# Kernel optimization log

Measured on AMD Instinct MI355X. Metric: run time of the kernel, lower is better.

Reference implementation:

```python
import jax, jax.numpy as jnp
import numpy as np

NUM_CLASSES = 80
REG_MAX = 16
CLS_W, BOX_W, DFL_W = 1.0, 2.5, 0.5


def _make_anchors(img=640, strides=(8, 16, 32)):
    pts, strs = [], []
    for s in strides:
        n = img // s
        xs = (np.arange(n, dtype=np.float32) + 0.5) * s
        gy, gx = np.meshgrid(xs, xs, indexing='ij')
        pts.append(np.stack([gx.ravel(), gy.ravel()], axis=1))
        strs.append(np.full((n * n, 1), float(s), np.float32))
    return np.concatenate(pts, 0).astype(np.float32), np.concatenate(strs, 0)


def setup_inputs() -> dict:
    key = jax.random.key(0)
    k1, k2, k3, k4, k5 = jax.random.split(key, 5)
    B, G = 16, 20
    ap, st = _make_anchors()  # A = 8400
    A = ap.shape[0]
    cls_scores = jax.random.uniform(k1, (B, A, NUM_CLASSES), dtype=jnp.float32)
    reg_distri = jax.random.normal(k2, (B, A, 4 * (REG_MAX + 1)), dtype=jnp.float32)
    cxcy = jax.random.uniform(k3, (B, G, 2), dtype=jnp.float32) * 560.0 + 40.0
    wh = jax.random.uniform(k4, (B, G, 2), dtype=jnp.float32) * 120.0 + 20.0
    gt_boxes = jnp.concatenate([cxcy - wh * 0.5, cxcy + wh * 0.5], axis=-1)  # xyxy
    gt_labels = jax.random.randint(k5, (B, G), 0, NUM_CLASSES)
    return {"cls_scores": cls_scores, "reg_distri": reg_distri, "gt_boxes": gt_boxes,
            "anchor_points": jnp.asarray(ap), "stride_tensor": jnp.asarray(st),
            "gt_labels": gt_labels}


def _per_image(pred_cls, pred_reg, gt_boxes, gt_labels, anchor_points, stride):
    A, C = pred_cls.shape
    G = gt_boxes.shape[0]
    k = max(min(13, A // max(G, 1)), 3)
    p = jnp.clip(pred_cls, 1e-7, 1.0 - 1e-7)
    centers = (gt_boxes[:, :2] + gt_boxes[:, 2:]) * 0.5                    # [G,2]
    d = jnp.sqrt(jnp.sum((anchor_points[:, None, :] - centers[None]) ** 2, -1))  # [A,G]
    _, topk_idx = jax.lax.top_k(-d.T, k)                                    # [G,k] nearest anchors
    ax = anchor_points[topk_idx]                                            # [G,k,2]
    inside = ((ax[..., 0] >= gt_boxes[:, None, 0]) & (ax[..., 0] <= gt_boxes[:, None, 2]) &
              (ax[..., 1] >= gt_boxes[:, None, 1]) & (ax[..., 1] <= gt_boxes[:, None, 3]))
    any_in = inside.any(-1, keepdims=True)
    assign_k = jnp.where(any_in, inside, jnp.arange(k) < 3)                 # fallback: 3 nearest
    assign = jnp.zeros((G, A), bool).at[jnp.arange(G)[:, None], topk_idx].set(assign_k)
    aT = assign.T                                                           # [A,G]
    fg = aT.any(1)                                                          # [A]
    last_gt = (G - 1) - jnp.argmax(aT[:, ::-1], axis=1)
    target_box = jnp.where(fg[:, None], gt_boxes[last_gt], 0.0)             # [A,4]
    onehot = jax.nn.one_hot(gt_labels, C, dtype=p.dtype)                    # [G,C]
    target_cls = jnp.max(aT[:, :, None].astype(p.dtype) * onehot[None], axis=1)  # [A,C]
    bce = -(target_cls * jnp.log(p) + (1.0 - target_cls) * jnp.log(1.0 - p))
    num_pos = fg.sum().astype(p.dtype)
    pos_w = jnp.minimum(A / jnp.maximum(num_pos, 1.0), 50.0)
    fgf = fg.astype(p.dtype)[:, None]
    pos_loss = jnp.where(num_pos > 0,
                         jnp.sum(bce * fgf) / jnp.maximum(num_pos * C, 1.0) * pos_w, 0.0)
    neg_loss = jnp.sum(bce * (1.0 - fgf)) / jnp.maximum((A - num_pos) * C, 1.0)
    # box decode (DFL expectation) + smooth-L1 on fg anchors
    reg = jax.nn.softmax(pred_reg.reshape(A, 4, REG_MAX + 1), axis=-1)
    proj = jnp.arange(REG_MAX + 1, dtype=p.dtype)
    dist = jnp.sum(reg * proj, axis=-1)                                     # [A,4]
    s = stride[:, 0]
    pb = jnp.stack([anchor_points[:, 0] - dist[:, 0] * s,
                    anchor_points[:, 1] - dist[:, 1] * s,
                    anchor_points[:, 0] + dist[:, 2] * s,
                    anchor_points[:, 1] + dist[:, 3] * s], axis=-1)
    diff = pb - target_box
    ad = jnp.abs(diff)
    sl1 = jnp.where(ad < 1.0, 0.5 * diff * diff, ad - 0.5)
    box_loss = jnp.where(num_pos > 0,
                         jnp.sum(sl1 * fgf) / jnp.maximum(num_pos * 4.0, 1.0), 0.0)
    return pos_loss + neg_loss, box_loss


def reference(cls_scores, reg_distri, gt_boxes, anchor_points, stride_tensor, gt_labels):
    cls_l, box_l = jax.vmap(
        lambda pc, pr, gb, gl: _per_image(pc, pr, gb, gl, anchor_points, stride_tensor)
    )(cls_scores, reg_distri, gt_boxes, gt_labels)
    loss_cls = cls_l.mean() * CLS_W
    loss_box = box_l.mean() * BOX_W
    return loss_cls + loss_box  # loss_dfl is identically 0 in the original
```

## Files before the change

kernel.cpp:

```cpp
#include <hip/hip_runtime.h>
#include <hip/hip_bf16.h>
#include <cfloat>

#define C_NUM 80
#define REG_MAXP1 17
#define NS 33
#define MAXA 8448
#define FG_STRIDE 512

__device__ inline void cand_for_slot(int sc, float cx, float cy, float& v, int& idx)
{
    v = FLT_MAX; idx = 0x7fffffff;
    int loc, w, n, strd, base;
    if (sc < 36)      { loc = sc;      w = 6; n = 80; strd = 8;  base = 0; }
    else if (sc < 52) { loc = sc - 36; w = 4; n = 40; strd = 16; base = 6400; }
    else if (sc < 68) { loc = sc - 52; w = 4; n = 20; strd = 32; base = 8000; }
    else return;
    float inv = 1.0f / (float)strd;
    int ix0 = (int)floorf(cx * inv - 0.5f) - (w / 2 - 1);
    int iy0 = (int)floorf(cy * inv - 0.5f) - (w / 2 - 1);
    int ix = ix0 + loc % w, iy = iy0 + loc / w;
    if (ix < 0 || ix >= n || iy < 0 || iy >= n) return;
    float ax = ((float)ix + 0.5f) * (float)strd;
    float ay = ((float)iy + 0.5f) * (float)strd;
    float dx = ax - cx, dy = ay - cy;
    v = dx * dx + dy * dy;
    idx = base + iy * n + ix;
}

__global__ __launch_bounds__(1024) void assignraster_kernel(const float* __restrict__ gt_boxes,
                              unsigned int* __restrict__ mask,
                              int* __restrict__ fglist,
                              int* __restrict__ npos,
                              float* __restrict__ acc,
                              int A, int G, int k)
{
    __shared__ unsigned int lmask[8400];
    __shared__ int s_cnt;
    int b = blockIdx.x, t = threadIdx.x;
    int wv = t >> 6, lane = t & 63;

    for (int i = t; i < A; i += 1024) lmask[i] = 0u;
    if (t == 0) s_cnt = 0;
    if (t < 3) acc[b * 3 + t] = 0.f;
    __syncthreads();

    for (int g = wv; g < G; g += 16) {
        const float* box = gt_boxes + (size_t)(b * G + g) * 4;
        float x0 = box[0], y0 = box[1], x1 = box[2], y1 = box[3];
        float cx = (x0 + x1) * 0.5f, cy = (y0 + y1) * 0.5f;

        float v0, v1; int i0, i1;
        cand_for_slot(lane,      cx, cy, v0, i0);
        cand_for_slot(lane + 64, cx, cy, v1, i1);

        int my_sel = 0x7fffffff;
        for (int it = 0; it < k; ++it) {
            float lb; int li; bool s0;
            if (v0 < v1 || (v0 == v1 && i0 < i1)) { lb = v0; li = i0; s0 = true; }
            else                                   { lb = v1; li = i1; s0 = false; }
            float rb = lb; int ri = li;
            for (int off = 32; off; off >>= 1) {
                float ov = __shfl_down(rb, off);
                int   oi = __shfl_down(ri, off);
                if (ov < rb || (ov == rb && oi < ri)) { rb = ov; ri = oi; }
            }
            int win = __shfl(ri, 0);
            if (lane == it) my_sel = win;
            if (li == win) {
                if (s0) { v0 = FLT_MAX; i0 = 0x7fffffff; }
                else    { v1 = FLT_MAX; i1 = 0x7fffffff; }
            }
        }

        bool inside = false;
        if (lane < k && my_sel < 0x7fffffff) {
            int idx = my_sel, n, strd, base;
            if (idx < 6400)      { n = 80; strd = 8;  base = 0; }
            else if (idx < 8000) { n = 40; strd = 16; base = 6400; }
            else                 { n = 20; strd = 32; base = 8000; }
            int loc = idx - base;
            float ax = ((float)(loc % n) + 0.5f) * (float)strd;
            float ay = ((float)(loc / n) + 0.5f) * (float)strd;
            inside = (ax >= x0) && (ax <= x1) && (ay >= y0) && (ay <= y1);
        }
        unsigned long long ball = __ballot(inside);
        if (lane < k && my_sel < 0x7fffffff) {
            bool asg = ball ? inside : (lane < 3);
            if (asg) atomicOr(&lmask[my_sel], 1u << g);
        }
    }
    __syncthreads();

    for (int i = t; i < A; i += 1024) {
        unsigned int m = lmask[i];
        mask[(size_t)b * A + i] = m;
        bool fg = (m != 0u);
        unsigned long long bal = __ballot(fg);
        int cnt = __popcll(bal);
        int base = 0;
        if (lane == 0 && cnt) base = atomicAdd(&s_cnt, cnt);
        base = __shfl(base, 0);
        if (fg) {
            int pre = __popcll(bal & ((1ull << lane) - 1ull));
            fglist[b * FG_STRIDE + base + pre] = i | ((31 - __clz(m)) << 16);
        }
    }
    __syncthreads();
    if (t == 0) npos[b] = s_cnt;
}

__global__ __launch_bounds__(256) void assign_kernel(const float* __restrict__ gt_boxes,
                              const float* __restrict__ anchor_points,
                              int* __restrict__ sel,
                              int B, int A, int G, int k)
{
    __shared__ float s_val[4];
    __shared__ int   s_idx[4];
    __shared__ int   s_sel;
    __shared__ int   s_topk[16];
    __shared__ int   s_anyin;

    int bg = blockIdx.x;
    int b = bg / G, g = bg % G;
    const float* box = gt_boxes + (size_t)(b * G + g) * 4;
    float x0 = box[0], y0 = box[1], x1 = box[2], y1 = box[3];
    float cx = (x0 + x1) * 0.5f, cy = (y0 + y1) * 0.5f;

    int t = threadIdx.x;
    float dv[NS];
#pragma unroll
    for (int s = 0; s < NS; ++s) {
        int i = t + s * 256;
        float d = FLT_MAX;
        if (i < A) {
            float dx = anchor_points[2 * i] - cx;
            float dy = anchor_points[2 * i + 1] - cy;
            d = dx * dx + dy * dy;
        }
        dv[s] = d;
    }

    int wid = t >> 6, lane = t & 63;
    for (int it = 0; it < k; ++it) {
        float best = FLT_MAX; int bi = 0x7fffffff;
#pragma unroll
        for (int s = 0; s < NS; ++s) {
            if (dv[s] < best) { best = dv[s]; bi = t + s * 256; }
        }
        for (int off = 32; off; off >>= 1) {
            float ov = __shfl_down(best, off);
            int   oi = __shfl_down(bi, off);
            if (ov < best || (ov == best && oi < bi)) { best = ov; bi = oi; }
        }
        if (lane == 0) { s_val[wid] = best; s_idx[wid] = bi; }
        __syncthreads();
        if (t == 0) {
            float bv = s_val[0]; int bix = s_idx[0];
#pragma unroll
            for (int w = 1; w < 4; ++w) {
                if (s_val[w] < bv || (s_val[w] == bv && s_idx[w] < bix)) { bv = s_val[w]; bix = s_idx[w]; }
            }
            s_sel = bix;
            s_topk[it] = bix;
        }
        __syncthreads();
        int selx = s_sel;
        if ((selx & 255) == t) {
            int slot = selx >> 8;
#pragma unroll
            for (int s = 0; s < NS; ++s) if (s == slot) dv[s] = FLT_MAX;
        }
    }

    if (t == 0) s_anyin = 0;
    __syncthreads();
    bool inside = false; int aidx = -1;
    if (t < k) {
        aidx = s_topk[t];
        float ax = anchor_points[2 * aidx], ay = anchor_points[2 * aidx + 1];
        inside = (ax >= x0) && (ax <= x1) && (ay >= y0) && (ay <= y1);
        if (inside) atomicOr(&s_anyin, 1);
    }
    __syncthreads();
    if (t < k) {
        bool asg = s_anyin ? inside : (t < 3);
        sel[(size_t)bg * 16 + t] = asg ? aidx : -1;
    }
}

__global__ __launch_bounds__(256) void raster_kernel(const int* __restrict__ sel,
                              unsigned int* __restrict__ mask,
                              int* __restrict__ fglist,
                              int* __restrict__ npos,
                              float* __restrict__ acc,
                              int A, int G, int k)
{
    __shared__ unsigned int lmask[MAXA];
    __shared__ int s_cnt;
    int b = blockIdx.x, t = threadIdx.x;

    for (int i = t; i < A; i += 256) lmask[i] = 0u;
    if (t == 0) s_cnt = 0;
    if (t < 3) acc[b * 3 + t] = 0.f;
    __syncthreads();

    for (int i = t; i < G * 16; i += 256) {
        int slot = i & 15;
        if (slot < k) {
            int a = sel[(size_t)(b * G) * 16 + i];
            if (a >= 0) atomicOr(&lmask[a], 1u << (i >> 4));
        }
    }
    __syncthreads();

    for (int i = t; i < A; i += 256) {
        unsigned int m = lmask[i];
        mask[(size_t)b * A + i] = m;
        if (m) {
            int lg = 31 - __clz(m);
            int p = atomicAdd(&s_cnt, 1);
            fglist[b * FG_STRIDE + p] = i | (lg << 16);
        }
    }
    __syncthreads();
    if (t == 0) npos[b] = s_cnt;
}

__global__ __launch_bounds__(256) void clsbox_kernel(const float4* __restrict__ cls,
                           const float* __restrict__ reg,
                           const float* __restrict__ gt_boxes,
                           const float* __restrict__ ap,
                           const float* __restrict__ st,
                           const unsigned int* __restrict__ mask,
                           const int* __restrict__ gt_labels,
                           const int* __restrict__ fglist,
                           const int* __restrict__ npos,
                           float* __restrict__ acc, int A, int G)
{
    const int CQ = C_NUM / 4;
    int b = blockIdx.y;
    int nq = A * CQ;
    const float4* base = cls + (size_t)b * nq;
    const unsigned int* mrow = mask + (size_t)b * A;
    const int* lab = gt_labels + (size_t)b * G;

    float pos = 0.f, neg = 0.f;
    for (int q = blockIdx.x * 256 + threadIdx.x; q < nq; q += gridDim.x * 256) {
        float4 v = base[q];
        unsigned int m = mrow[q / CQ];
        float p0 = fminf(fmaxf(v.x, 1e-7f), 1.0f - 1e-7f);
        float p1 = fminf(fmaxf(v.y, 1e-7f), 1.0f - 1e-7f);
        float p2 = fminf(fmaxf(v.z, 1e-7f), 1.0f - 1e-7f);
        float p3 = fminf(fmaxf(v.w, 1e-7f), 1.0f - 1e-7f);
        if (m) {
            int c0 = (q % CQ) * 4;
            unsigned int tm = 0, mm = m;
            while (mm) {
                int g = __ffs(mm) - 1;
                mm &= mm - 1;
                unsigned int d = (unsigned int)(lab[g] - c0);
                if (d < 4u) tm |= 1u << d;
            }
            pos -= __logf((tm & 1u) ? p0 : 1.0f - p0);
            pos -= __logf((tm & 2u) ? p1 : 1.0f - p1);
            pos -= __logf((tm & 4u) ? p2 : 1.0f - p2);
            pos -= __logf((tm & 8u) ? p3 : 1.0f - p3);
        } else {
            neg -= __logf(1.0f - p0) + __logf(1.0f - p1) + __logf(1.0f - p2) + __logf(1.0f - p3);
        }
    }

    float bx = 0.f;
    int e = blockIdx.x * 256 + threadIdx.x;
    if (e < npos[b]) {
        int ent = fglist[b * FG_STRIDE + e];
        int a = ent & 0xffff;
        int lg = ent >> 16;
        const float* tb = gt_boxes + (size_t)(b * G + lg) * 4;
        const float* r = reg + ((size_t)b * A + a) * (4 * REG_MAXP1);
        float s = st[a];
        float axp = ap[2 * a], ayp = ap[2 * a + 1];
#pragma unroll
        for (int j = 0; j < 4; ++j) {
            const float* rj = r + j * REG_MAXP1;
            float rr[REG_MAXP1];
#pragma unroll
            for (int i = 0; i < REG_MAXP1; ++i) rr[i] = rj[i];
            float mx = rr[0];
#pragma unroll
            for (int i = 1; i < REG_MAXP1; ++i) mx = fmaxf(mx, rr[i]);
            float sum = 0.f, dot = 0.f;
#pragma unroll
            for (int i = 0; i < REG_MAXP1; ++i) {
                float ev = __expf(rr[i] - mx);
                sum += ev; dot += ev * (float)i;
            }
            float dist = dot / sum;
            float pbj = (j < 2) ? ((j == 0 ? axp : ayp) - dist * s)
                                : ((j == 2 ? axp : ayp) + dist * s);
            float df = pbj - tb[j];
            float ad = fabsf(df);
            bx += (ad < 1.0f) ? 0.5f * df * df : ad - 0.5f;
        }
    }

    for (int off = 32; off; off >>= 1) {
        pos += __shfl_down(pos, off);
        neg += __shfl_down(neg, off);
        bx  += __shfl_down(bx, off);
    }
    __shared__ float sp[4], sn[4], sb[4];
    int wid = threadIdx.x >> 6, lane = threadIdx.x & 63;
    if (lane == 0) { sp[wid] = pos; sn[wid] = neg; sb[wid] = bx; }
    __syncthreads();
    if (threadIdx.x == 0) {
        float P = sp[0] + sp[1] + sp[2] + sp[3];
        float N = sn[0] + sn[1] + sn[2] + sn[3];
        float X = sb[0] + sb[1] + sb[2] + sb[3];
        if (P != 0.f) atomicAdd(&acc[b * 3 + 0], P);
        if (N != 0.f) atomicAdd(&acc[b * 3 + 1], N);
        if (X != 0.f) atomicAdd(&acc[b * 3 + 2], X);
    }
}

__global__ void final_kernel(const float* __restrict__ acc,
                             const int* __restrict__ npos,
                             float* __restrict__ out, int B, int A)
{
    if (threadIdx.x == 0 && blockIdx.x == 0) {
        float cls_sum = 0.f, box_sum = 0.f;
        for (int b = 0; b < B; ++b) {
            float np = (float)npos[b];
            float neg = acc[b * 3 + 1] / fmaxf(((float)A - np) * (float)C_NUM, 1.0f);
            float pos = 0.f, box = 0.f;
            if (np > 0.f) {
                float pw = fminf((float)A / fmaxf(np, 1.0f), 50.0f);
                pos = acc[b * 3 + 0] / fmaxf(np * (float)C_NUM, 1.0f) * pw;
                box = acc[b * 3 + 2] / fmaxf(np * 4.0f, 1.0f);
            }
            cls_sum += pos + neg;
            box_sum += box;
        }
        out[0] = cls_sum / (float)B * 1.0f + box_sum / (float)B * 2.5f;
    }
}

extern "C" void kernel_launch(void* const* d_in, const int* in_sizes, int n_in,
                              void* d_out, int out_size, void* d_ws, size_t ws_size,
                              hipStream_t stream)
{
    const float* cls   = (const float*)d_in[0];
    const float* reg   = (const float*)d_in[1];
    const float* gtb   = (const float*)d_in[2];
    const float* ap    = (const float*)d_in[3];
    const float* st    = (const float*)d_in[4];
    const int*   glab  = (const int*)d_in[5];

    int A = in_sizes[3] / 2;
    int B = in_sizes[0] / (A * C_NUM);
    int G = in_sizes[5] / B;
    int k = A / (G > 1 ? G : 1); if (k > 13) k = 13; if (k < 3) k = 3;

    unsigned int* mask = (unsigned int*)d_ws;
    float* acc   = (float*)(mask + (size_t)B * A);
    int*   npos  = (int*)(acc + 3 * B);
    int*   sel   = npos + B;
    int*   fgl   = sel + (size_t)B * G * 16;

    if (A == 8400 && G <= 32) {
        assignraster_kernel<<<B, 1024, 0, stream>>>(gtb, mask, fgl, npos, acc, A, G, k);
    } else {
        assign_kernel<<<B * G, 256, 0, stream>>>(gtb, ap, sel, B, A, G, k);
        raster_kernel<<<B, 256, 0, stream>>>(sel, mask, fgl, npos, acc, A, G, k);
    }

    dim3 g3(128, B);
    clsbox_kernel<<<g3, 256, 0, stream>>>((const float4*)cls, reg, gtb, ap, st,
                                          mask, glab, fgl, npos, acc, A, G);

    final_kernel<<<1, 64, 0, stream>>>(acc, npos, (float*)d_out, B, A);
}
```

Measured before the change: 159.9 us.

## Split cls and box loss into separate kernels, unroll cls loop by two

Splits the fused cls/box kernel into a streaming BCE kernel and a separate foreground box kernel that gives each of the four box sides its own thread. The cls loop now issues two float4 loads per iteration to raise memory-level parallelism. Removing the serial box work from the first blocks of the cls grid avoids a tail where those blocks run longer than the rest. The cost is one extra kernel launch and a second pass to reduce the box loss.

```diff
diff --git a/kernel.cpp b/kernel.cpp
--- a/kernel.cpp
+++ b/kernel.cpp
@@ -227,15 +227,33 @@
     if (t == 0) npos[b] = s_cnt;
 }
 
-__global__ __launch_bounds__(256) void clsbox_kernel(const float4* __restrict__ cls,
-                           const float* __restrict__ reg,
-                           const float* __restrict__ gt_boxes,
-                           const float* __restrict__ ap,
-                           const float* __restrict__ st,
+__device__ inline void bce4(float4 v, unsigned int m, const int* __restrict__ lab,
+                            int c0, float& pos, float& neg)
+{
+    float p0 = fminf(fmaxf(v.x, 1e-7f), 1.0f - 1e-7f);
+    float p1 = fminf(fmaxf(v.y, 1e-7f), 1.0f - 1e-7f);
+    float p2 = fminf(fmaxf(v.z, 1e-7f), 1.0f - 1e-7f);
+    float p3 = fminf(fmaxf(v.w, 1e-7f), 1.0f - 1e-7f);
+    if (m) {
+        unsigned int tm = 0, mm = m;
+        while (mm) {
+            int g = __ffs(mm) - 1;
+            mm &= mm - 1;
+            unsigned int d = (unsigned int)(lab[g] - c0);
+            if (d < 4u) tm |= 1u << d;
+        }
+        pos -= __logf((tm & 1u) ? p0 : 1.0f - p0);
+        pos -= __logf((tm & 2u) ? p1 : 1.0f - p1);
+        pos -= __logf((tm & 4u) ? p2 : 1.0f - p2);
+        pos -= __logf((tm & 8u) ? p3 : 1.0f - p3);
+    } else {
+        neg -= __logf(1.0f - p0) + __logf(1.0f - p1) + __logf(1.0f - p2) + __logf(1.0f - p3);
+    }
+}
+
+__global__ __launch_bounds__(256) void cls_kernel(const float4* __restrict__ cls,
                            const unsigned int* __restrict__ mask,
                            const int* __restrict__ gt_labels,
-                           const int* __restrict__ fglist,
-                           const int* __restrict__ npos,
                            float* __restrict__ acc, int A, int G)
 {
     const int CQ = C_NUM / 4;
@@ -244,82 +262,81 @@
     const float4* base = cls + (size_t)b * nq;
     const unsigned int* mrow = mask + (size_t)b * A;
     const int* lab = gt_labels + (size_t)b * G;
+    int stride = gridDim.x * 256;
 
     float pos = 0.f, neg = 0.f;
-    for (int q = blockIdx.x * 256 + threadIdx.x; q < nq; q += gridDim.x * 256) {
-        float4 v = base[q];
-        unsigned int m = mrow[q / CQ];
-        float p0 = fminf(fmaxf(v.x, 1e-7f), 1.0f - 1e-7f);
-        float p1 = fminf(fmaxf(v.y, 1e-7f), 1.0f - 1e-7f);
-        float p2 = fminf(fmaxf(v.z, 1e-7f), 1.0f - 1e-7f);
-        float p3 = fminf(fmaxf(v.w, 1e-7f), 1.0f - 1e-7f);
-        if (m) {
-            int c0 = (q % CQ) * 4;
-            unsigned int tm = 0, mm = m;
-            while (mm) {
-                int g = __ffs(mm) - 1;
-                mm &= mm - 1;
-                unsigned int d = (unsigned int)(lab[g] - c0);
-                if (d < 4u) tm |= 1u << d;
-            }
-            pos -= __logf((tm & 1u) ? p0 : 1.0f - p0);
-            pos -= __logf((tm & 2u) ? p1 : 1.0f - p1);
-            pos -= __logf((tm & 4u) ? p2 : 1.0f - p2);
-            pos -= __logf((tm & 8u) ? p3 : 1.0f - p3);
-        } else {
-            neg -= __logf(1.0f - p0) + __logf(1.0f - p1) + __logf(1.0f - p2) + __logf(1.0f - p3);
-        }
-    }
-
+    for (int q0 = blockIdx.x * 256 + threadIdx.x; q0 < nq; q0 += 2 * stride) {
+        int q1 = q0 + stride;
+        bool h1 = q1 < nq;
+        float4 va = base[q0];
+        unsigned int ma = mrow[q0 / CQ];
+        float4 vb; unsigned int mb = 0;
+        if (h1) { vb = base[q1]; mb = mrow[q1 / CQ]; }
+        bce4(va, ma, lab, (q0 % CQ) * 4, pos, neg);
+        if (h1) bce4(vb, mb, lab, (q1 % CQ) * 4, pos, neg);
+    }
+
+    for (int off = 32; off; off >>= 1) {
+        pos += __shfl_down(pos, off);
+        neg += __shfl_down(neg, off);
+    }
+    __shared__ float sp[4], sn[4];
+    int wid = threadIdx.x >> 6, lane = threadIdx.x & 63;
+    if (lane == 0) { sp[wid] = pos; sn[wid] = neg; }
+    __syncthreads();
+    if (threadIdx.x == 0) {
+        float P = sp[0] + sp[1] + sp[2] + sp[3];
+        float N = sn[0] + sn[1] + sn[2] + sn[3];
+        if (P != 0.f) atomicAdd(&acc[b * 3 + 0], P);
+        if (N != 0.f) atomicAdd(&acc[b * 3 + 1], N);
+    }
+}
+
+__global__ __launch_bounds__(256) void boxfg_kernel(const float* __restrict__ reg,
+                           const float* __restrict__ gt_boxes,
+                           const float* __restrict__ ap,
+                           const float* __restrict__ st,
+                           const int* __restrict__ fglist,
+                           const int* __restrict__ npos,
+                           float* __restrict__ acc, int A, int G)
+{
+    int b = blockIdx.y;
+    int idx = blockIdx.x * 256 + threadIdx.x;
+    int e = idx >> 2, j = idx & 3;
     float bx = 0.f;
-    int e = blockIdx.x * 256 + threadIdx.x;
     if (e < npos[b]) {
         int ent = fglist[b * FG_STRIDE + e];
         int a = ent & 0xffff;
         int lg = ent >> 16;
-        const float* tb = gt_boxes + (size_t)(b * G + lg) * 4;
-        const float* r = reg + ((size_t)b * A + a) * (4 * REG_MAXP1);
+        float tbj = gt_boxes[(size_t)(b * G + lg) * 4 + j];
+        const float* rj = reg + ((size_t)b * A + a) * (4 * REG_MAXP1) + j * REG_MAXP1;
+        float rr[REG_MAXP1];
+#pragma unroll
+        for (int i = 0; i < REG_MAXP1; ++i) rr[i] = rj[i];
+        float mx = rr[0];
+#pragma unroll
+        for (int i = 1; i < REG_MAXP1; ++i) mx = fmaxf(mx, rr[i]);
+        float sum = 0.f, dot = 0.f;
+#pragma unroll
+        for (int i = 0; i < REG_MAXP1; ++i) {
+            float ev = __expf(rr[i] - mx);
+            sum += ev; dot += ev * (float)i;
+        }
+        float dist = dot / sum;
         float s = st[a];
-        float axp = ap[2 * a], ayp = ap[2 * a + 1];
-#pragma unroll
-        for (int j = 0; j < 4; ++j) {
-            const float* rj = r + j * REG_MAXP1;
-            float rr[REG_MAXP1];
-#pragma unroll
-            for (int i = 0; i < REG_MAXP1; ++i) rr[i] = rj[i];
-            float mx = rr[0];
-#pragma unroll
-            for (int i = 1; i < REG_MAXP1; ++i) mx = fmaxf(mx, rr[i]);
-            float sum = 0.f, dot = 0.f;
-#pragma unroll
-            for (int i = 0; i < REG_MAXP1; ++i) {
-                float ev = __expf(rr[i] - mx);
-                sum += ev; dot += ev * (float)i;
-            }
-            float dist = dot / sum;
-            float pbj = (j < 2) ? ((j == 0 ? axp : ayp) - dist * s)
-                                : ((j == 2 ? axp : ayp) + dist * s);
-            float df = pbj - tb[j];
-            float ad = fabsf(df);
-            bx += (ad < 1.0f) ? 0.5f * df * df : ad - 0.5f;
-        }
-    }
-
-    for (int off = 32; off; off >>= 1) {
-        pos += __shfl_down(pos, off);
-        neg += __shfl_down(neg, off);
-        bx  += __shfl_down(bx, off);
-    }
-    __shared__ float sp[4], sn[4], sb[4];
+        float ac = ap[2 * a + (j & 1)];
+        float pbj = (j < 2) ? (ac - dist * s) : (ac + dist * s);
+        float df = pbj - tbj;
+        float ad = fabsf(df);
+        bx = (ad < 1.0f) ? 0.5f * df * df : ad - 0.5f;
+    }
+    for (int off = 32; off; off >>= 1) bx += __shfl_down(bx, off);
+    __shared__ float sb[4];
     int wid = threadIdx.x >> 6, lane = threadIdx.x & 63;
-    if (lane == 0) { sp[wid] = pos; sn[wid] = neg; sb[wid] = bx; }
+    if (lane == 0) sb[wid] = bx;
     __syncthreads();
     if (threadIdx.x == 0) {
-        float P = sp[0] + sp[1] + sp[2] + sp[3];
-        float N = sn[0] + sn[1] + sn[2] + sn[3];
         float X = sb[0] + sb[1] + sb[2] + sb[3];
-        if (P != 0.f) atomicAdd(&acc[b * 3 + 0], P);
-        if (N != 0.f) atomicAdd(&acc[b * 3 + 1], N);
         if (X != 0.f) atomicAdd(&acc[b * 3 + 2], X);
     }
 }
@@ -376,8 +393,10 @@
     }
 
     dim3 g3(128, B);
-    clsbox_kernel<<<g3, 256, 0, stream>>>((const float4*)cls, reg, gtb, ap, st,
-                                          mask, glab, fgl, npos, acc, A, G);
+    cls_kernel<<<g3, 256, 0, stream>>>((const float4*)cls, mask, glab, acc, A, G);
+
+    dim3 g4((FG_STRIDE * 4 + 255) / 256, B);
+    boxfg_kernel<<<g4, 256, 0, stream>>>(reg, gtb, ap, st, fgl, npos, acc, A, G);
 
     final_kernel<<<1, 64, 0, stream>>>(acc, npos, (float*)d_out, B, A);
 }
```

Measured after the change: 154.8 us. -3.2%, faster.
